# Kernel tuning notes

Hardware: AMD Instinct MI355X
Metric: run time of the kernel (lower is better)

Reference implementation:

```python
import jax, jax.numpy as jnp
import numpy as np

N_NODES = 50000
N_EDGES = 800000
D_IN = 128
D_HID = 128
D_OUT = 128


def _gcn_layer(x, W, b, src, dst, norm):
    # dense projection then edge-weighted gather -> scatter-add at dst
    h = x @ W                                   # [N, d_out]
    msg = h[src] * norm[:, None]                # [E, d_out]
    out = jax.ops.segment_sum(msg, dst, num_segments=N_NODES)
    return out + b


def setup_inputs() -> dict:
    key = jax.random.key(0)
    k = jax.random.split(key, 8)
    x = jax.random.normal(k[0], (N_NODES, D_IN), dtype=jnp.float32)
    edge_index = jax.random.randint(k[1], (2, N_EDGES), 0, N_NODES, dtype=jnp.int64)
    edge_weight = jax.random.uniform(k[2], (N_EDGES,), dtype=jnp.float32)
    # GCNConv params (glorot-ish scale)
    s1 = 1.0 / np.sqrt(D_IN)
    s2 = 1.0 / np.sqrt(D_HID)
    W1 = jax.random.normal(k[3], (D_IN, D_HID), dtype=jnp.float32) * s1
    b1 = jnp.zeros((D_HID,), dtype=jnp.float32)
    W2 = jax.random.normal(k[4], (D_HID, D_OUT), dtype=jnp.float32) * s2
    b2 = jnp.zeros((D_OUT,), dtype=jnp.float32)
    return {"x": x, "edge_index": edge_index, "edge_weight": edge_weight,
            "W1": W1, "b1": b1, "W2": W2, "b2": b2}


def reference(x, edge_index, edge_weight, W1, b1, W2, b2):
    src, dst = edge_index[0], edge_index[1]
    # gcn_norm (add_self_loops=False): deg from scatter-add of edge_weight at dst
    deg = jax.ops.segment_sum(edge_weight, dst, num_segments=N_NODES)
    dinv = jnp.where(deg > 0, jax.lax.rsqrt(jnp.maximum(deg, 1e-30)), 0.0)
    norm = dinv[src] * edge_weight * dinv[dst]  # [E]
    h = jax.nn.relu(_gcn_layer(x, W1, b1, src, dst, norm))
    out = _gcn_layer(h, W2, b2, src, dst, norm)
    # F.dropout in eval mode (deterministic reference) is identity
    return out
```

## Files before the change

### kernel.cpp

```cpp
#include <hip/hip_runtime.h>

#define N_NODES 50000
#define N_EDGES 800000
#define D 128
#define MAXDEG 64
#define NBUCK 196
#define BUCKCAP 5120
#define EPB 4096
#define NBB 196
#define SP 136

typedef __attribute__((ext_vector_type(8))) short bf16x8;
typedef __attribute__((ext_vector_type(4))) float f32x4;

__device__ inline unsigned short f2bf(float f) {
    unsigned u = __float_as_uint(f);
    unsigned r = (u + 0x7fffu + ((u >> 16) & 1u)) >> 16;
    return (unsigned short)r;
}

__global__ __launch_bounds__(256) void k_bucket(const int* __restrict__ src,
                                                const int* __restrict__ dst,
                                                const float* __restrict__ ew,
                                                int* __restrict__ cursor,
                                                uint2* __restrict__ buck,
                                                const float* __restrict__ W1,
                                                const float* __restrict__ W2,
                                                unsigned short* __restrict__ Wt1,
                                                unsigned short* __restrict__ Wt2) {
    if (blockIdx.x >= NBB) {
        const float* W = (blockIdx.x == NBB) ? W1 : W2;
        unsigned short* Wt = (blockIdx.x == NBB) ? Wt1 : Wt2;
        for (int idx = threadIdx.x; idx < D * D; idx += 256) {
            int n = idx & 127, k = idx >> 7;
            Wt[n * D + k] = f2bf(W[k * D + n]);
        }
        return;
    }
    __shared__ uint2 sorted[EPB];
    __shared__ int hist[NBUCK];
    __shared__ int scn[NBUCK];
    __shared__ int gbase[NBUCK];
    __shared__ int s[256];
    int tid = threadIdx.x;
    int e0 = blockIdx.x * EPB;
    for (int i = tid; i < NBUCK; i += 256) hist[i] = 0;
    __syncthreads();
    #pragma unroll
    for (int j = 0; j < 16; ++j) {
        int e = e0 + j * 256 + tid;
        if (e < N_EDGES) atomicAdd(&hist[dst[e] >> 8], 1);
    }
    __syncthreads();
    int v = tid < NBUCK ? hist[tid] : 0;
    s[tid] = v;
    __syncthreads();
    for (int off = 1; off < 256; off <<= 1) {
        int u = tid >= off ? s[tid - off] : 0;
        __syncthreads();
        s[tid] += u;
        __syncthreads();
    }
    int excl = s[tid] - v;
    if (tid < NBUCK) {
        scn[tid] = excl;
        gbase[tid] = v ? atomicAdd(&cursor[tid], v) : 0;
        hist[tid] = excl;
    }
    __syncthreads();
    #pragma unroll
    for (int j = 0; j < 16; ++j) {
        int e = e0 + j * 256 + tid;
        if (e < N_EDGES) {
            int d = dst[e];
            int sv = src[e];
            unsigned wf = min(__float2uint_rn(ew[e] * 65536.f), 65535u);
            int slot = atomicAdd(&hist[d >> 8], 1);
            sorted[slot] = make_uint2(((unsigned)sv << 16) | wf, (unsigned)d);
        }
    }
    __syncthreads();
    int total = min(EPB, N_EDGES - e0);
    for (int i = tid; i < total; i += 256) {
        uint2 en = sorted[i];
        int bk = (int)(en.y >> 8);
        int g = gbase[bk] + (i - scn[bk]);
        if (g < BUCKCAP)
            buck[(size_t)bk * BUCKCAP + g] = make_uint2(en.x, en.y & 255u);
    }
}

#define GB 782
__global__ __launch_bounds__(256) void k_build_gemm(
        const int* __restrict__ cursor, const uint2* __restrict__ buck,
        unsigned* __restrict__ csr, int* __restrict__ cnt,
        float* __restrict__ dinv,
        const float* __restrict__ X, const unsigned short* __restrict__ Wt1,
        unsigned short* __restrict__ h0) {
    __shared__ union SM {
        struct {
            unsigned csr_loc[256 * MAXDEG];
            int cnt_loc[256];
            int deg_loc[256];
        } b;
        unsigned short sX[64 * D];
    } sm;
    int tid = threadIdx.x;

    if (blockIdx.x < NBUCK) {
        int b = blockIdx.x;
        sm.b.cnt_loc[tid] = 0;
        sm.b.deg_loc[tid] = 0;
        {
            uint4* z4 = (uint4*)sm.b.csr_loc;
            #pragma unroll
            for (int i = 0; i < (256 * MAXDEG / 4) / 256; ++i)
                z4[i * 256 + tid] = make_uint4(0u, 0u, 0u, 0u);
        }
        __syncthreads();
        int n = min(cursor[b], BUCKCAP);
        const uint2* bb = buck + (size_t)b * BUCKCAP;
        for (int i = tid; i < n; i += 256) {
            uint2 e = bb[i];
            int ln = e.y;
            int slot = atomicAdd(&sm.b.cnt_loc[ln], 1);
            if (slot < MAXDEG) sm.b.csr_loc[ln * MAXDEG + slot] = e.x;
            atomicAdd(&sm.b.deg_loc[ln], (int)(e.x & 0xffffu));
        }
        __syncthreads();
        int node0 = b * 256;
        int nnodes = min(256, N_NODES - node0);
        uint4* g = (uint4*)(csr + (size_t)node0 * MAXDEG);
        const uint4* l = (const uint4*)sm.b.csr_loc;
        int nv = nnodes * (MAXDEG / 4);
        for (int i = tid; i < nv; i += 256) g[i] = l[i];
        if (tid < nnodes) {
            int node = node0 + tid;
            cnt[node] = min(sm.b.cnt_loc[tid], MAXDEG);
            float sum = (float)sm.b.deg_loc[tid] * (1.f / 65536.f);
            dinv[node] = sum > 0.f ? rsqrtf(fmaxf(sum, 1e-30f)) : 0.f;
        }
        return;
    }

    int row0 = (blockIdx.x - NBUCK) * 64;
    int nr = min(64, N_NODES - row0);
    {
        const float4* xs = (const float4*)(X + (size_t)row0 * D);
        int nvec = nr * (D / 4);
        for (int i = tid; i < nvec; i += 256) {
            float4 v = xs[i];
            ushort4 o;
            o.x = f2bf(v.x); o.y = f2bf(v.y); o.z = f2bf(v.z); o.w = f2bf(v.w);
            *(ushort4*)(sm.sX + i * 4) = o;
        }
    }
    __syncthreads();

    int wave = tid >> 6, lane = tid & 63;
    int m = lane & 15, quad = lane >> 4;
    f32x4 acc[8];
    #pragma unroll
    for (int i = 0; i < 8; ++i) acc[i] = (f32x4){0.f, 0.f, 0.f, 0.f};

    const unsigned short* aBase = sm.sX + (wave * 16 + m) * D + quad * 8;
    #pragma unroll
    for (int c = 0; c < 4; ++c) {
        bf16x8 a = *(const bf16x8*)(aBase + c * 32);
        #pragma unroll
        for (int n0 = 0; n0 < 8; ++n0) {
            bf16x8 b = *(const bf16x8*)(Wt1 + (n0 * 16 + m) * D + c * 32 + quad * 8);
            acc[n0] = __builtin_amdgcn_mfma_f32_16x16x32_bf16(a, b, acc[n0], 0, 0, 0);
        }
    }

    unsigned short* sOut = sm.sX + wave * 16 * D;
    __syncthreads();
    #pragma unroll
    for (int n0 = 0; n0 < 8; ++n0)
        #pragma unroll
        for (int i = 0; i < 4; ++i)
            sOut[(quad * 4 + i) * D + n0 * 16 + m] = f2bf(acc[n0][i]);
    __syncthreads();
    int rr = lane >> 2, c0 = (lane & 3) * 32;
    int grow = row0 + wave * 16 + rr;
    if (grow < N_NODES) {
        uint4* dstp = (uint4*)(h0 + (size_t)grow * D + c0);
        const uint4* srcp = (const uint4*)(sOut + rr * D + c0);
        dstp[0] = srcp[0]; dstp[1] = srcp[1]; dstp[2] = srcp[2]; dstp[3] = srcp[3];
    }
}

__global__ __launch_bounds__(256) void k_agg_mm(const unsigned short* __restrict__ H,
                                                const int* __restrict__ cnt,
                                                const unsigned* __restrict__ csr,
                                                const float* __restrict__ dinv,
                                                const float* __restrict__ b1,
                                                const unsigned short* __restrict__ Wt2,
                                                unsigned short* __restrict__ Hb) {
    __shared__ unsigned short sT[16 * SP];
    int tid = threadIdx.x, wave = tid >> 6, lane = tid & 63;
    int g = lane >> 4, fl = lane & 15;
    int nb = blockIdx.x * 16;

    for (int nn = 0; nn < 4; ++nn) {
        int node = nb + wave * 4 + nn;
        const uint4* row4 = (const uint4*)(csr + (size_t)node * MAXDEG);
        int end = min(cnt[node], MAXDEG);
        int nw = (end + 15) >> 4;
        uint4 c4[4];
        #pragma unroll
        for (int w = 0; w < 4; ++w) c4[w] = row4[w * 4 + g];
        float acc[8] = {0.f, 0.f, 0.f, 0.f, 0.f, 0.f, 0.f, 0.f};
        #pragma unroll
        for (int w = 0; w < 4; ++w) {
            if (w < nw) {
                unsigned cs[4] = {c4[w].x, c4[w].y, c4[w].z, c4[w].w};
                uint4 u[4];
                float nmv[4];
                #pragma unroll
                for (int j = 0; j < 4; ++j) {
                    unsigned sv = cs[j] >> 16;
                    u[j] = *(const uint4*)(H + (size_t)sv * D + fl * 8);
                    nmv[j] = (float)(cs[j] & 0xffffu) * (1.f / 65536.f)
                             * dinv[sv];
                }
                #pragma unroll
                for (int j = 0; j < 4; ++j) {
                    unsigned a0[4] = {u[j].x, u[j].y, u[j].z, u[j].w};
                    #pragma unroll
                    for (int q = 0; q < 4; ++q) {
                        acc[2 * q]     += __uint_as_float(a0[q] << 16) * nmv[j];
                        acc[2 * q + 1] += __uint_as_float(a0[q] & 0xffff0000u) * nmv[j];
                    }
                }
            }
        }
        #pragma unroll
        for (int j = 0; j < 8; ++j) {
            acc[j] += __shfl_xor(acc[j], 16, 64);
            acc[j] += __shfl_xor(acc[j], 32, 64);
        }
        if (g < 2) {
            float dn = dinv[node];
            int f = fl * 8 + g * 4;
            ushort4 o;
            o.x = f2bf(fmaxf(acc[g * 4 + 0] * dn + b1[f + 0], 0.f));
            o.y = f2bf(fmaxf(acc[g * 4 + 1] * dn + b1[f + 1], 0.f));
            o.z = f2bf(fmaxf(acc[g * 4 + 2] * dn + b1[f + 2], 0.f));
            o.w = f2bf(fmaxf(acc[g * 4 + 3] * dn + b1[f + 3], 0.f));
            *(ushort4*)(sT + (wave * 4 + nn) * SP + f) = o;
        }
    }
    __syncthreads();

    int m = lane & 15, quad = lane >> 4;
    f32x4 acc2[2];
    acc2[0] = (f32x4){0.f, 0.f, 0.f, 0.f};
    acc2[1] = (f32x4){0.f, 0.f, 0.f, 0.f};
    #pragma unroll
    for (int c = 0; c < 4; ++c) {
        bf16x8 a = *(const bf16x8*)(sT + m * SP + c * 32 + quad * 8);
        #pragma unroll
        for (int t = 0; t < 2; ++t) {
            int n0 = wave * 2 + t;
            bf16x8 b = *(const bf16x8*)(Wt2 + (n0 * 16 + m) * D + c * 32 + quad * 8);
            acc2[t] = __builtin_amdgcn_mfma_f32_16x16x32_bf16(a, b, acc2[t], 0, 0, 0);
        }
    }
    float dv[4];
    #pragma unroll
    for (int i = 0; i < 4; ++i) dv[i] = dinv[nb + quad * 4 + i];
    __syncthreads();
    #pragma unroll
    for (int t = 0; t < 2; ++t)
        #pragma unroll
        for (int i = 0; i < 4; ++i)
            sT[(quad * 4 + i) * SP + (wave * 2 + t) * 16 + m] = f2bf(acc2[t][i] * dv[i]);
    __syncthreads();
    int rr = tid >> 4, cc = (tid & 15) * 8;
    *(uint4*)(Hb + (size_t)(nb + rr) * D + cc) = *(const uint4*)(sT + rr * SP + cc);
}

__global__ __launch_bounds__(256) void k_aggregate(const unsigned short* __restrict__ H,
                                                   const int* __restrict__ cnt,
                                                   const unsigned* __restrict__ csr,
                                                   const float* __restrict__ dinv,
                                                   const float* __restrict__ bias,
                                                   float* __restrict__ out) {
    int node = blockIdx.x * 4 + (threadIdx.x >> 6);
    int lane = threadIdx.x & 63;
    int g = lane >> 4;
    int fl = lane & 15;
    const uint4* row4 = (const uint4*)(csr + (size_t)node * MAXDEG);
    int end = min(cnt[node], MAXDEG);
    int nw = (end + 15) >> 4;
    uint4 c4[4];
    #pragma unroll
    for (int w = 0; w < 4; ++w) c4[w] = row4[w * 4 + g];
    float acc[8] = {0.f, 0.f, 0.f, 0.f, 0.f, 0.f, 0.f, 0.f};
    #pragma unroll
    for (int w = 0; w < 4; ++w) {
        if (w < nw) {
            unsigned cs[4] = {c4[w].x, c4[w].y, c4[w].z, c4[w].w};
            uint4 u[4];
            float nmv[4];
            #pragma unroll
            for (int j = 0; j < 4; ++j) {
                unsigned sv = cs[j] >> 16;
                u[j] = *(const uint4*)(H + (size_t)sv * D + fl * 8);
                nmv[j] = (float)(cs[j] & 0xffffu) * (1.f / 65536.f);
            }
            #pragma unroll
            for (int j = 0; j < 4; ++j) {
                unsigned a0[4] = {u[j].x, u[j].y, u[j].z, u[j].w};
                #pragma unroll
                for (int q = 0; q < 4; ++q) {
                    acc[2 * q]     += __uint_as_float(a0[q] << 16) * nmv[j];
                    acc[2 * q + 1] += __uint_as_float(a0[q] & 0xffff0000u) * nmv[j];
                }
            }
        }
    }
    #pragma unroll
    for (int j = 0; j < 8; ++j) {
        acc[j] += __shfl_xor(acc[j], 16, 64);
        acc[j] += __shfl_xor(acc[j], 32, 64);
    }
    if (g < 2) {
        float dn = dinv[node];
        int f = fl * 8 + g * 4;
        *(float4*)(out + (size_t)node * D + f) =
            make_float4(acc[g * 4 + 0] * dn + bias[f + 0],
                        acc[g * 4 + 1] * dn + bias[f + 1],
                        acc[g * 4 + 2] * dn + bias[f + 2],
                        acc[g * 4 + 3] * dn + bias[f + 3]);
    }
}

extern "C" void kernel_launch(void* const* d_in, const int* in_sizes, int n_in,
                              void* d_out, int out_size, void* d_ws, size_t ws_size,
                              hipStream_t stream) {
    const float* x   = (const float*)d_in[0];
    const int*   ei  = (const int*)d_in[1];
    const float* ew  = (const float*)d_in[2];
    const float* W1  = (const float*)d_in[3];
    const float* b1  = (const float*)d_in[4];
    const float* W2  = (const float*)d_in[5];
    const float* b2  = (const float*)d_in[6];
    float* out = (float*)d_out;

    const int* src = ei;
    const int* dst = ei + N_EDGES;

    char* base = (char*)d_ws;
    size_t off = 0;
    auto take = [&](size_t bytes) -> char* {
        char* p = base + off;
        off += (bytes + 255) & ~(size_t)255;
        return p;
    };
    int*      cursor = (int*)take(NBUCK * 4);
    size_t zero_bytes = off;
    float*    dinv = (float*)take(N_NODES * 4);
    int*      cnt  = (int*)take(N_NODES * 4);
    uint2*    buck = (uint2*)take((size_t)NBUCK * BUCKCAP * 8);
    unsigned* csr  = (unsigned*)take((size_t)N_NODES * MAXDEG * 4);
    unsigned short* Wt1 = (unsigned short*)take(D * D * 2);
    unsigned short* Wt2 = (unsigned short*)take(D * D * 2);
    unsigned short* h0  = (unsigned short*)take((size_t)N_NODES * D * 2);
    unsigned short* hb  = (unsigned short*)take((size_t)N_NODES * D * 2);

    hipMemsetAsync(d_ws, 0, zero_bytes, stream);

    const int FB = N_NODES / 16;
    const int AB = N_NODES / 4;

    k_bucket<<<NBB + 2, 256, 0, stream>>>(src, dst, ew, cursor, buck,
                                          W1, W2, Wt1, Wt2);
    k_build_gemm<<<NBUCK + GB, 256, 0, stream>>>(cursor, buck, csr, cnt, dinv,
                                                 x, Wt1, h0);
    k_agg_mm<<<FB, 256, 0, stream>>>(h0, cnt, csr, dinv, b1, Wt2, hb);
    k_aggregate<<<AB, 256, 0, stream>>>(hb, cnt, csr, dinv, b2, out);
}
```

Measured before the change: 197.9 us.

## Assign one node per 16-lane group in aggregation kernels instead of per wave

Both aggregation kernels now map each 16-lane quarter-wave to its own node, with each lane owning 8 features, and loop over that node's edges in chunks of 8. Before, a whole wave handled one node, splitting edges across four lane groups and then combining them with cross-lane shuffles. The new mapping drops the shuffle reduction and the idle lanes in the epilogue, and it runs a dynamic loop bounded by the node's degree instead of a fixed unrolled 4×16 pattern. In exchange, each lane handles more edges one after another and has fewer gathers in flight per edge, and lanes in a wave can diverge when their nodes have different degrees. The chunk loop can also read CSR padding slots past the node's degree, which are only safe if they hold zero-weight entries.

```diff
diff --git a/kernel.cpp b/kernel.cpp
--- a/kernel.cpp
+++ b/kernel.cpp
@@ -202,55 +202,50 @@
     int tid = threadIdx.x, wave = tid >> 6, lane = tid & 63;
     int g = lane >> 4, fl = lane & 15;
     int nb = blockIdx.x * 16;
-
-    for (int nn = 0; nn < 4; ++nn) {
-        int node = nb + wave * 4 + nn;
-        const uint4* row4 = (const uint4*)(csr + (size_t)node * MAXDEG);
-        int end = min(cnt[node], MAXDEG);
-        int nw = (end + 15) >> 4;
-        uint4 c4[4];
-        #pragma unroll
-        for (int w = 0; w < 4; ++w) c4[w] = row4[w * 4 + g];
-        float acc[8] = {0.f, 0.f, 0.f, 0.f, 0.f, 0.f, 0.f, 0.f};
-        #pragma unroll
-        for (int w = 0; w < 4; ++w) {
-            if (w < nw) {
-                unsigned cs[4] = {c4[w].x, c4[w].y, c4[w].z, c4[w].w};
-                uint4 u[4];
-                float nmv[4];
-                #pragma unroll
-                for (int j = 0; j < 4; ++j) {
-                    unsigned sv = cs[j] >> 16;
-                    u[j] = *(const uint4*)(H + (size_t)sv * D + fl * 8);
-                    nmv[j] = (float)(cs[j] & 0xffffu) * (1.f / 65536.f)
-                             * dinv[sv];
-                }
-                #pragma unroll
-                for (int j = 0; j < 4; ++j) {
-                    unsigned a0[4] = {u[j].x, u[j].y, u[j].z, u[j].w};
-                    #pragma unroll
-                    for (int q = 0; q < 4; ++q) {
-                        acc[2 * q]     += __uint_as_float(a0[q] << 16) * nmv[j];
-                        acc[2 * q + 1] += __uint_as_float(a0[q] & 0xffff0000u) * nmv[j];
-                    }
-                }
+    int node = nb + wave * 4 + g;
+
+    int end = min(cnt[node], MAXDEG);
+    const uint4* row4 = (const uint4*)(csr + (size_t)node * MAXDEG);
+    float acc[8] = {0.f, 0.f, 0.f, 0.f, 0.f, 0.f, 0.f, 0.f};
+    for (int b0 = 0; b0 < end; b0 += 8) {
+        uint4 ca = row4[(b0 >> 2)];
+        uint4 cb = row4[(b0 >> 2) + 1];
+        unsigned cs[8] = {ca.x, ca.y, ca.z, ca.w, cb.x, cb.y, cb.z, cb.w};
+        uint4 u[8];
+        float nmv[8];
+        #pragma unroll
+        for (int j = 0; j < 8; ++j) {
+            unsigned sv = cs[j] >> 16;
+            u[j] = *(const uint4*)(H + (size_t)sv * D + fl * 8);
+            nmv[j] = (float)(cs[j] & 0xffffu) * (1.f / 65536.f) * dinv[sv];
+        }
+        #pragma unroll
+        for (int j = 0; j < 8; ++j) {
+            unsigned a0[4] = {u[j].x, u[j].y, u[j].z, u[j].w};
+            #pragma unroll
+            for (int q = 0; q < 4; ++q) {
+                acc[2 * q]     += __uint_as_float(a0[q] << 16) * nmv[j];
+                acc[2 * q + 1] += __uint_as_float(a0[q] & 0xffff0000u) * nmv[j];
             }
         }
-        #pragma unroll
-        for (int j = 0; j < 8; ++j) {
-            acc[j] += __shfl_xor(acc[j], 16, 64);
-            acc[j] += __shfl_xor(acc[j], 32, 64);
-        }
-        if (g < 2) {
-            float dn = dinv[node];
-            int f = fl * 8 + g * 4;
-            ushort4 o;
-            o.x = f2bf(fmaxf(acc[g * 4 + 0] * dn + b1[f + 0], 0.f));
-            o.y = f2bf(fmaxf(acc[g * 4 + 1] * dn + b1[f + 1], 0.f));
-            o.z = f2bf(fmaxf(acc[g * 4 + 2] * dn + b1[f + 2], 0.f));
-            o.w = f2bf(fmaxf(acc[g * 4 + 3] * dn + b1[f + 3], 0.f));
-            *(ushort4*)(sT + (wave * 4 + nn) * SP + f) = o;
-        }
+    }
+    {
+        float dn = dinv[node];
+        int f = fl * 8;
+        float4 bv0 = *(const float4*)(b1 + f);
+        float4 bv1 = *(const float4*)(b1 + f + 4);
+        ushort4 o0, o1;
+        o0.x = f2bf(fmaxf(acc[0] * dn + bv0.x, 0.f));
+        o0.y = f2bf(fmaxf(acc[1] * dn + bv0.y, 0.f));
+        o0.z = f2bf(fmaxf(acc[2] * dn + bv0.z, 0.f));
+        o0.w = f2bf(fmaxf(acc[3] * dn + bv0.w, 0.f));
+        o1.x = f2bf(fmaxf(acc[4] * dn + bv1.x, 0.f));
+        o1.y = f2bf(fmaxf(acc[5] * dn + bv1.y, 0.f));
+        o1.z = f2bf(fmaxf(acc[6] * dn + bv1.z, 0.f));
+        o1.w = f2bf(fmaxf(acc[7] * dn + bv1.w, 0.f));
+        unsigned short* tp = sT + (wave * 4 + g) * SP + f;
+        *(ushort4*)(tp) = o0;
+        *(ushort4*)(tp + 4) = o1;
     }
     __syncthreads();
 
@@ -288,54 +283,44 @@
                                                    const float* __restrict__ dinv,
                                                    const float* __restrict__ bias,
                                                    float* __restrict__ out) {
-    int node = blockIdx.x * 4 + (threadIdx.x >> 6);
-    int lane = threadIdx.x & 63;
-    int g = lane >> 4;
-    int fl = lane & 15;
+    int tid = threadIdx.x, wave = tid >> 6, lane = tid & 63;
+    int g = lane >> 4, fl = lane & 15;
+    int node = blockIdx.x * 16 + wave * 4 + g;
+
+    int end = min(cnt[node], MAXDEG);
     const uint4* row4 = (const uint4*)(csr + (size_t)node * MAXDEG);
-    int end = min(cnt[node], MAXDEG);
-    int nw = (end + 15) >> 4;
-    uint4 c4[4];
-    #pragma unroll
-    for (int w = 0; w < 4; ++w) c4[w] = row4[w * 4 + g];
     float acc[8] = {0.f, 0.f, 0.f, 0.f, 0.f, 0.f, 0.f, 0.f};
-    #pragma unroll
-    for (int w = 0; w < 4; ++w) {
-        if (w < nw) {
-            unsigned cs[4] = {c4[w].x, c4[w].y, c4[w].z, c4[w].w};
-            uint4 u[4];
-            float nmv[4];
+    for (int b0 = 0; b0 < end; b0 += 8) {
+        uint4 ca = row4[(b0 >> 2)];
+        uint4 cb = row4[(b0 >> 2) + 1];
+        unsigned cs[8] = {ca.x, ca.y, ca.z, ca.w, cb.x, cb.y, cb.z, cb.w};
+        uint4 u[8];
+        float nmv[8];
+        #pragma unroll
+        for (int j = 0; j < 8; ++j) {
+            unsigned sv = cs[j] >> 16;
+            u[j] = *(const uint4*)(H + (size_t)sv * D + fl * 8);
+            nmv[j] = (float)(cs[j] & 0xffffu) * (1.f / 65536.f);
+        }
+        #pragma unroll
+        for (int j = 0; j < 8; ++j) {
+            unsigned a0[4] = {u[j].x, u[j].y, u[j].z, u[j].w};
             #pragma unroll
-            for (int j = 0; j < 4; ++j) {
-                unsigned sv = cs[j] >> 16;
-                u[j] = *(const uint4*)(H + (size_t)sv * D + fl * 8);
-                nmv[j] = (float)(cs[j] & 0xffffu) * (1.f / 65536.f);
+            for (int q = 0; q < 4; ++q) {
+                acc[2 * q]     += __uint_as_float(a0[q] << 16) * nmv[j];
+                acc[2 * q + 1] += __uint_as_float(a0[q] & 0xffff0000u) * nmv[j];
             }
-            #pragma unroll
-            for (int j = 0; j < 4; ++j) {
-                unsigned a0[4] = {u[j].x, u[j].y, u[j].z, u[j].w};
-                #pragma unroll
-                for (int q = 0; q < 4; ++q) {
-                    acc[2 * q]     += __uint_as_float(a0[q] << 16) * nmv[j];
-                    acc[2 * q + 1] += __uint_as_float(a0[q] & 0xffff0000u) * nmv[j];
-                }
-            }
-        }
-    }
-    #pragma unroll
-    for (int j = 0; j < 8; ++j) {
-        acc[j] += __shfl_xor(acc[j], 16, 64);
-        acc[j] += __shfl_xor(acc[j], 32, 64);
-    }
-    if (g < 2) {
-        float dn = dinv[node];
-        int f = fl * 8 + g * 4;
-        *(float4*)(out + (size_t)node * D + f) =
-            make_float4(acc[g * 4 + 0] * dn + bias[f + 0],
-                        acc[g * 4 + 1] * dn + bias[f + 1],
-                        acc[g * 4 + 2] * dn + bias[f + 2],
-                        acc[g * 4 + 3] * dn + bias[f + 3]);
-    }
+        }
+    }
+    float dn = dinv[node];
+    int f = fl * 8;
+    float4 bv0 = *(const float4*)(bias + f);
+    float4 bv1 = *(const float4*)(bias + f + 4);
+    float* op = out + (size_t)node * D + f;
+    *(float4*)(op) = make_float4(acc[0] * dn + bv0.x, acc[1] * dn + bv0.y,
+                                 acc[2] * dn + bv0.z, acc[3] * dn + bv0.w);
+    *(float4*)(op + 4) = make_float4(acc[4] * dn + bv1.x, acc[5] * dn + bv1.y,
+                                     acc[6] * dn + bv1.z, acc[7] * dn + bv1.w);
 }
 
 extern "C" void kernel_launch(void* const* d_in, const int* in_sizes, int n_in,
@@ -374,7 +359,7 @@
     hipMemsetAsync(d_ws, 0, zero_bytes, stream);
 
     const int FB = N_NODES / 16;
-    const int AB = N_NODES / 4;
+    const int AB = N_NODES / 16;
 
     k_bucket<<<NBB + 2, 256, 0, stream>>>(src, dst, ew, cursor, buck,
                                           W1, W2, Wt1, Wt2);
```

Result: no change. 194.9 us (-1.5%).
